# Kernel optimization log

Measured on AMD Instinct MI355X. Metric: run time of the kernel, lower is better.

Reference implementation:

```python
import jax, jax.numpy as jnp
import numpy as np

B, T, C, D = 64, 4096, 51, 64
MASK_PROB = 0.3
LN_EPS = 1e-5


def setup_inputs() -> dict:
    key = jax.random.key(0)
    k0, k1, k2, k3, k4 = jax.random.split(key, 5)
    x = jax.random.normal(k0, (B, T, C), dtype=jnp.float32)
    # xavier_uniform_ then *= 0.5 (as in reset_parameters)
    bound = float(np.sqrt(6.0 / (C + D)))
    W = jax.random.uniform(k1, (C, D), jnp.float32, -bound, bound) * 0.5
    Wm = jax.random.uniform(k2, (C, D), jnp.float32, -bound, bound) * 0.5
    gamma = jnp.ones((D,), jnp.float32)
    beta = jnp.zeros((D,), jnp.float32)
    time_mask = jax.random.bernoulli(k3, MASK_PROB, (B, T))
    sensor_mask = jax.random.bernoulli(k4, MASK_PROB, (B, C))
    return {"x": x, "W": W, "Wm": Wm, "gamma": gamma, "beta": beta,
            "time_mask": time_mask, "sensor_mask": sensor_mask}


def reference(x, W, Wm, gamma, beta, time_mask, sensor_mask):
    # mask[b,t,c] = time_mask[b,t] OR sensor_mask[b,c]
    mask = (time_mask[:, :, None] | sensor_mask[:, None, :]).astype(x.dtype)  # [B,T,C]
    # Fused masked reductions (math-equivalent to the broadcast [B,T,C,D] path)
    xu = jnp.einsum('btc,cd->btd', x * (1.0 - mask), W)   # [B,T,D]
    xm = jnp.einsum('btc,cd->btd', mask, Wm)              # [B,T,D]
    out = xu + xm
    # LayerNorm over last dim
    mu = jnp.mean(out, axis=-1, keepdims=True)
    var = jnp.mean((out - mu) ** 2, axis=-1, keepdims=True)
    out = (out - mu) * jax.lax.rsqrt(var + LN_EPS) * gamma + beta
    return out
```

## Files before the change

kernel.cpp:

```cpp
#include <hip/hip_runtime.h>

#define BB 64
#define TT 4096
#define CC 51
#define DD 64
#define LN_EPS 1e-5f

typedef __attribute__((ext_vector_type(8))) short short8;
typedef __attribute__((ext_vector_type(4))) float f32x4;

union FragU { int i[4]; short8 s; };

#define DPP_QP_1032   0xB1
#define DPP_QP_2301   0x4E
#define DPP_ROW_HMIRR 0x141
#define DPP_ROW_MIRR  0x140

__device__ __forceinline__ float dpp_add(float v, int tag) {
  int t;
  switch (tag) {
    case 0: t = __builtin_amdgcn_update_dpp(0, __float_as_int(v), DPP_QP_1032,   0xF, 0xF, true); break;
    case 1: t = __builtin_amdgcn_update_dpp(0, __float_as_int(v), DPP_QP_2301,   0xF, 0xF, true); break;
    case 2: t = __builtin_amdgcn_update_dpp(0, __float_as_int(v), DPP_ROW_HMIRR, 0xF, 0xF, true); break;
    default: t = __builtin_amdgcn_update_dpp(0, __float_as_int(v), DPP_ROW_MIRR, 0xF, 0xF, true); break;
  }
  return v + __int_as_float(t);
}
__device__ __forceinline__ float allsum16(float v) {
  v = dpp_add(v, 0); v = dpp_add(v, 1); v = dpp_add(v, 2); v = dpp_add(v, 3);
  return v;
}
__device__ __forceinline__ float allsum64(float v) {
  v = allsum16(v);
  v += __shfl_xor(v, 16, 64);
  v += __shfl_xor(v, 32, 64);
  return v;
}

__device__ __forceinline__ int pack_hl(float x) {
  const unsigned u = __float_as_uint(x);
  const unsigned h = u >> 16;
  const float hf = __uint_as_float(u & 0xFFFF0000u);
  const unsigned l = __float_as_uint(x - hf) >> 16;
  return (int)(h | (l << 16));
}

__global__ void ipmask_setup2(const float* __restrict__ Wm,
                              const float* __restrict__ gamma,
                              const float* __restrict__ beta,
                              const int* __restrict__ smask,
                              float* __restrict__ ws) {
  const int b = blockIdx.x, d = threadIdx.x;
  float bs = 0.0f, f = 0.0f;
  for (int c = 0; c < CC; ++c) {
    const float wmv = Wm[c * DD + d];
    const float sf = (float)smask[b * CC + c];
    bs = fmaf(sf, wmv, bs);
    f += wmv;
  }
  ws[b * 128 + d] = bs;
  const float s1 = allsum64(f);
  const float s2 = allsum64(f * f);
  const float mu = s1 * (1.0f / 64.0f);
  const float vr = fmaf(-mu, mu, s2 * (1.0f / 64.0f));
  const float rs = rsqrtf(vr + LN_EPS);
  ws[b * 128 + 64 + d] = fmaf((f - mu) * rs, gamma[d], beta[d]);
}

__global__ __launch_bounds__(256, 4)
void ipmask_mfma2(const float* __restrict__ x, const float* __restrict__ W,
                  const float* __restrict__ gamma, const float* __restrict__ beta,
                  const int* __restrict__ tmask, const int* __restrict__ smask,
                  const float* __restrict__ ws, float* __restrict__ out) {
  const int t = threadIdx.x, L = t & 63;
  const int q = L >> 4, m16 = L & 15;
  const int gw = (blockIdx.x << 2) + (t >> 6);
  const int b = gw >> 6;
  const int rowBase = (b << 12) + ((gw & 63) << 6);

  const int* smB = smask + b * CC;

  f32x4 acc[4][4];
#pragma unroll
  for (int nt = 0; nt < 4; ++nt) {
    const float bias_nt = ws[b * 128 + nt * 16 + m16];
#pragma unroll
    for (int mt = 0; mt < 4; ++mt) {
      acc[mt][nt][0] = bias_nt; acc[mt][nt][1] = bias_nt;
      acc[mt][nt][2] = bias_nt; acc[mt][nt][3] = bias_nt;
    }
  }

#pragma unroll
  for (int ks = 0; ks < 4; ++ks) {
    FragU bmu[4], bcu[4];
#pragma unroll
    for (int j = 0; j < 4; ++j) {
      const int c = ks * 16 + q * 4 + j;
      const int smv = (c < CC) ? smB[c] : 1;
#pragma unroll
      for (int nt = 0; nt < 4; ++nt) {
        const int n = nt * 16 + m16;
        float we = 0.0f;
        if (c < CC) we = W[c * DD + n];
        if (smv) we = 0.0f;
        const unsigned u = __float_as_uint(we);
        const unsigned h = u >> 16;
        const float hf = __uint_as_float(u & 0xFFFF0000u);
        const unsigned l = __float_as_uint(we - hf) >> 16;
        bmu[nt].i[j] = (int)(h | (h << 16));
        bcu[nt].i[j] = (int)l;
      }
    }

#pragma unroll
    for (int mt = 0; mt < 4; ++mt) {
      const int row = rowBase + mt * 16 + m16;
      const float* xr = x + (size_t)row * CC;
      FragU au;
#pragma unroll
      for (int j = 0; j < 4; ++j) {
        const int c = ks * 16 + q * 4 + j;
        const float xv = (c < CC) ? xr[c] : 0.0f;
        au.i[j] = pack_hl(xv);
      }
#pragma unroll
      for (int nt = 0; nt < 4; ++nt) {
        acc[mt][nt] = __builtin_amdgcn_mfma_f32_16x16x32_bf16(au.s, bmu[nt].s, acc[mt][nt], 0, 0, 0);
        acc[mt][nt] = __builtin_amdgcn_mfma_f32_16x16x32_bf16(au.s, bcu[nt].s, acc[mt][nt], 0, 0, 0);
      }
    }
  }

  float g_[4], b_[4], cons_[4];
#pragma unroll
  for (int nt = 0; nt < 4; ++nt) {
    g_[nt] = gamma[nt * 16 + m16];
    b_[nt] = beta[nt * 16 + m16];
    cons_[nt] = ws[b * 128 + 64 + nt * 16 + m16];
  }
#pragma unroll
  for (int mt = 0; mt < 4; ++mt) {
#pragma unroll
    for (int rg = 0; rg < 4; ++rg) {
      float su = 0.0f, sq = 0.0f;
#pragma unroll
      for (int nt = 0; nt < 4; ++nt) {
        const float v = acc[mt][nt][rg];
        su += v;
        sq = fmaf(v, v, sq);
      }
      su = allsum16(su);
      sq = allsum16(sq);
      const float mu = su * (1.0f / 64.0f);
      const float vr = fmaf(-mu, mu, sq * (1.0f / 64.0f));
      const float rs = rsqrtf(vr + LN_EPS);
      const int row = rowBase + mt * 16 + q * 4 + rg;
      const int tm = tmask[row];
      const size_t obase = (size_t)row * DD;
#pragma unroll
      for (int nt = 0; nt < 4; ++nt) {
        float val = fmaf((acc[mt][nt][rg] - mu) * rs, g_[nt], b_[nt]);
        if (tm) val = cons_[nt];
        out[obase + nt * 16 + m16] = val;
      }
    }
  }
}

extern "C" void kernel_launch(void* const* d_in, const int* in_sizes, int n_in,
                              void* d_out, int out_size, void* d_ws, size_t ws_size,
                              hipStream_t stream) {
  const float* x     = (const float*)d_in[0];
  const float* W     = (const float*)d_in[1];
  const float* Wm    = (const float*)d_in[2];
  const float* gamma = (const float*)d_in[3];
  const float* beta  = (const float*)d_in[4];
  const int*   tmask = (const int*)d_in[5];
  const int*   smask = (const int*)d_in[6];
  float* out = (float*)d_out;
  float* ws  = (float*)d_ws;

  ipmask_setup2<<<dim3(BB), dim3(DD), 0, stream>>>(Wm, gamma, beta, smask, ws);
  ipmask_mfma2<<<dim3(1024), dim3(256), 0, stream>>>(
      x, W, gamma, beta, tmask, smask, ws, out);
}
```

Before: 154.2 us.

## Prefetch all x tile loads upfront and cache time mask in registers

The main kernel now loads its whole 64x51 x tile into registers before the MFMA loop, so all global loads are in flight together instead of being interleaved per k-step. It also loads the time mask once per lane and broadcasts it with shuffles, writes the output with nontemporal stores, and relaxes launch bounds to 2 blocks per SM to make room for the extra registers. The setup kernel splits its channel loop across four waves and combines the partial sums through shared memory. The risks are lower occupancy and higher register pressure, which could cut latency hiding.

Result: faster. 129.3 us (-16.2%).

```diff
diff --git a/kernel.cpp b/kernel.cpp
--- a/kernel.cpp
+++ b/kernel.cpp
@@ -45,30 +45,40 @@
   return (int)(h | (l << 16));
 }
 
-__global__ void ipmask_setup2(const float* __restrict__ Wm,
+__global__ void ipmask_setup3(const float* __restrict__ Wm,
                               const float* __restrict__ gamma,
                               const float* __restrict__ beta,
                               const int* __restrict__ smask,
                               float* __restrict__ ws) {
-  const int b = blockIdx.x, d = threadIdx.x;
+  __shared__ float red[8][64];
+  const int t = threadIdx.x, L = t & 63, w = t >> 6;
+  const int b = blockIdx.x;
+  const int c0 = w * 13, c1 = (c0 + 13 < CC) ? c0 + 13 : CC;
   float bs = 0.0f, f = 0.0f;
-  for (int c = 0; c < CC; ++c) {
-    const float wmv = Wm[c * DD + d];
+  for (int c = c0; c < c1; ++c) {
+    const float wmv = Wm[c * DD + L];
     const float sf = (float)smask[b * CC + c];
     bs = fmaf(sf, wmv, bs);
     f += wmv;
   }
-  ws[b * 128 + d] = bs;
-  const float s1 = allsum64(f);
-  const float s2 = allsum64(f * f);
-  const float mu = s1 * (1.0f / 64.0f);
-  const float vr = fmaf(-mu, mu, s2 * (1.0f / 64.0f));
-  const float rs = rsqrtf(vr + LN_EPS);
-  ws[b * 128 + 64 + d] = fmaf((f - mu) * rs, gamma[d], beta[d]);
-}
-
-__global__ __launch_bounds__(256, 4)
-void ipmask_mfma2(const float* __restrict__ x, const float* __restrict__ W,
+  red[w * 2][L] = bs;
+  red[w * 2 + 1][L] = f;
+  __syncthreads();
+  if (w == 0) {
+    bs = (red[0][L] + red[2][L]) + (red[4][L] + red[6][L]);
+    f  = (red[1][L] + red[3][L]) + (red[5][L] + red[7][L]);
+    ws[b * 128 + L] = bs;
+    const float s1 = allsum64(f);
+    const float s2 = allsum64(f * f);
+    const float mu = s1 * (1.0f / 64.0f);
+    const float vr = fmaf(-mu, mu, s2 * (1.0f / 64.0f));
+    const float rs = rsqrtf(vr + LN_EPS);
+    ws[b * 128 + 64 + L] = fmaf((f - mu) * rs, gamma[L], beta[L]);
+  }
+}
+
+__global__ __launch_bounds__(256, 2)
+void ipmask_mfma3(const float* __restrict__ x, const float* __restrict__ W,
                   const float* __restrict__ gamma, const float* __restrict__ beta,
                   const int* __restrict__ tmask, const int* __restrict__ smask,
                   const float* __restrict__ ws, float* __restrict__ out) {
@@ -79,6 +89,21 @@
   const int rowBase = (b << 12) + ((gw & 63) << 6);
 
   const int* smB = smask + b * CC;
+
+  float xf[4][4][4];
+#pragma unroll
+  for (int mt = 0; mt < 4; ++mt) {
+    const float* xr = x + (size_t)(rowBase + mt * 16 + m16) * CC;
+#pragma unroll
+    for (int ks = 0; ks < 4; ++ks) {
+#pragma unroll
+      for (int j = 0; j < 4; ++j) {
+        const int c = ks * 16 + q * 4 + j;
+        xf[mt][ks][j] = (c < CC) ? xr[c] : 0.0f;
+      }
+    }
+  }
+  const int tmv = tmask[rowBase + L];
 
   f32x4 acc[4][4];
 #pragma unroll
@@ -112,18 +137,11 @@
         bcu[nt].i[j] = (int)l;
       }
     }
-
 #pragma unroll
     for (int mt = 0; mt < 4; ++mt) {
-      const int row = rowBase + mt * 16 + m16;
-      const float* xr = x + (size_t)row * CC;
       FragU au;
 #pragma unroll
-      for (int j = 0; j < 4; ++j) {
-        const int c = ks * 16 + q * 4 + j;
-        const float xv = (c < CC) ? xr[c] : 0.0f;
-        au.i[j] = pack_hl(xv);
-      }
+      for (int j = 0; j < 4; ++j) au.i[j] = pack_hl(xf[mt][ks][j]);
 #pragma unroll
       for (int nt = 0; nt < 4; ++nt) {
         acc[mt][nt] = __builtin_amdgcn_mfma_f32_16x16x32_bf16(au.s, bmu[nt].s, acc[mt][nt], 0, 0, 0);
@@ -155,14 +173,14 @@
       const float mu = su * (1.0f / 64.0f);
       const float vr = fmaf(-mu, mu, sq * (1.0f / 64.0f));
       const float rs = rsqrtf(vr + LN_EPS);
-      const int row = rowBase + mt * 16 + q * 4 + rg;
-      const int tm = tmask[row];
-      const size_t obase = (size_t)row * DD;
+      const int rloc = mt * 16 + q * 4 + rg;
+      const int tm = __shfl(tmv, rloc, 64);
+      const size_t obase = (size_t)(rowBase + rloc) * DD;
 #pragma unroll
       for (int nt = 0; nt < 4; ++nt) {
         float val = fmaf((acc[mt][nt][rg] - mu) * rs, g_[nt], b_[nt]);
         if (tm) val = cons_[nt];
-        out[obase + nt * 16 + m16] = val;
+        __builtin_nontemporal_store(val, &out[obase + nt * 16 + m16]);
       }
     }
   }
@@ -181,7 +199,7 @@
   float* out = (float*)d_out;
   float* ws  = (float*)d_ws;
 
-  ipmask_setup2<<<dim3(BB), dim3(DD), 0, stream>>>(Wm, gamma, beta, smask, ws);
-  ipmask_mfma2<<<dim3(1024), dim3(256), 0, stream>>>(
+  ipmask_setup3<<<dim3(BB), dim3(256), 0, stream>>>(Wm, gamma, beta, smask, ws);
+  ipmask_mfma3<<<dim3(1024), dim3(256), 0, stream>>>(
       x, W, gamma, beta, tmask, smask, ws, out);
 }
```
